# Kernel tuning notes

Measured on AMD Instinct MI355X. Metric: run time of the kernel, lower is better.

Reference implementation:

```python
import jax, jax.numpy as jnp
import numpy as np

B, C_IN, C_OUT, H, W, K, NK = 16, 256, 256, 64, 64, 3, 2
EPS = 1e-8


def setup_inputs() -> dict:
    key = jax.random.key(0)
    k1, k2, k3, k4 = jax.random.split(key, 4)
    x = jax.random.normal(k1, (B, C_IN, H, W), dtype=jnp.float32)
    mod = jax.random.normal(k2, (B, C_IN), dtype=jnp.float32)
    kernel_mod = jax.random.normal(k3, (B, NK), dtype=jnp.float32)
    # kernel bank: [num_conv_kernels, dim_out, dim_in, k, k] (kaiming-ish scale)
    weights = jax.random.normal(k4, (NK, C_OUT, C_IN, K, K), dtype=jnp.float32) / np.sqrt(C_IN * K * K)
    gamma = jnp.ones((C_OUT,), dtype=jnp.float32)
    return {"x": x, "mod": mod, "kernel_mod": kernel_mod, "weights": weights, "gamma": gamma}


def _block(x, mod, kernel_mod, weights, gamma):
    # adaptive kernel selection: softmax-mix the kernel bank per sample
    attn = jax.nn.softmax(kernel_mod, axis=-1)                       # [b, n]
    w = jnp.einsum('bn,noikl->boikl', attn, weights)                 # [b, o, i, k, k]
    # style modulation over input channels
    w = w * (mod[:, None, :, None, None] + 1.0)
    # demodulation
    denom = jnp.clip(jnp.sum(w * w, axis=(2, 3, 4), keepdims=True), EPS)
    w = w * jax.lax.rsqrt(denom)
    # per-sample conv (groups=b trick in torch) -> vmap over batch
    def conv_one(fmap, wb):
        return jax.lax.conv_general_dilated(
            fmap[None], wb, window_strides=(1, 1), padding='SAME',
            dimension_numbers=('NCHW', 'OIHW', 'NCHW'))[0]
    y = jax.vmap(conv_one)(x, w)                                     # [b, o, h, w]
    # RMSNorm over channel dim: F.normalize(x, dim=1) * gamma * sqrt(dim)
    norm = jnp.sqrt(jnp.sum(y * y, axis=1, keepdims=True))
    y = y / jnp.maximum(norm, 1e-12)
    y = y * gamma[None, :, None, None] * (gamma.shape[0] ** 0.5)
    # SiLU
    return y * jax.nn.sigmoid(y)


def reference(x, mod, kernel_mod, weights, gamma):
    return _block(x, mod, kernel_mod, weights, gamma)
```

## Files before the change

kernel.cpp:

```cpp
#include <hip/hip_runtime.h>
#include <math.h>


typedef __attribute__((ext_vector_type(8))) short short8;
typedef __attribute__((ext_vector_type(16))) float f32x16;

#define GLL16(src, dst)                                                       \
  __builtin_amdgcn_global_load_lds(                                           \
      (const __attribute__((address_space(1))) unsigned int*)(src),           \
      (__attribute__((address_space(3))) unsigned int*)(dst), 16, 0, 0)

static __device__ __forceinline__ unsigned short f2bf(float v) {
  union { float f; unsigned u; } u;
  u.f = v;
  unsigned r = u.u + 0x7FFF + ((u.u >> 16) & 1);
  return (unsigned short)(r >> 16);
}

__global__ __launch_bounds__(256) void wprep(
    const float* __restrict__ mod, const float* __restrict__ kmod,
    const float* __restrict__ weights, unsigned short* __restrict__ wq) {
  int blk = blockIdx.x;
  int b = blk >> 5, oq = blk & 31;
  int t = threadIdx.x;
  int o_l = t >> 5, its = t & 31;
  int o = oq * 8 + o_l;

  float k0 = kmod[b * 2 + 0], k1 = kmod[b * 2 + 1];
  float mx = fmaxf(k0, k1);
  float e0 = expf(k0 - mx), e1 = expf(k1 - mx);
  float ai = 1.0f / (e0 + e1);
  float a0 = e0 * ai, a1 = e1 * ai;

  float wv[9][8];
  float s = 0.0f;
  const float* w0 = &weights[((size_t)o * 256 + its * 8) * 9];
  const float* w1 = w0 + 589824;
#pragma unroll
  for (int e = 0; e < 8; ++e) {
    float f = mod[b * 256 + its * 8 + e] + 1.0f;
#pragma unroll
    for (int j = 0; j < 9; ++j) {
      float v = (a0 * w0[e * 9 + j] + a1 * w1[e * 9 + j]) * f;
      wv[j][e] = v;
      s = fmaf(v, v, s);
    }
  }

  __shared__ float red[8][32];
  __shared__ float scl[8];
  red[o_l][its] = s;
  __syncthreads();
  if (t < 8) {
    float tot = 0.0f;
#pragma unroll
    for (int k = 0; k < 32; ++k) tot += red[t][k];
    scl[t] = rsqrtf(fmaxf(tot, 1e-8f));
  }
  __syncthreads();
  float sc = scl[o_l];

  int c = its >> 1, io = its & 1;
  int oh = o >> 7, mf = (o >> 5) & 3;
  int lane2 = (o & 31) + io * 32;
  size_t cbase = ((size_t)(b * 16 + c)) * 36864 + oh * 2048 + mf * 512 + lane2 * 8;
#pragma unroll
  for (int j = 0; j < 9; ++j) {
    short8 pk;
#pragma unroll
    for (int e = 0; e < 8; ++e) pk[e] = (short)f2bf(wv[j][e] * sc);
    *(short8*)(wq + cbase + j * 4096) = pk;
  }
}

__global__ __launch_bounds__(256) void xprep(
    const float* __restrict__ x, unsigned short* __restrict__ xq) {
  int blk = blockIdx.x;
  int rowp = blk % 66;
  int bc = blk / 66;
  int b = bc >> 4, c = bc & 15;
  int t = threadIdx.x;
  size_t obase = (size_t)blk * 1056;

  if (rowp == 0 || rowp == 65) {
    for (int idx = t; idx < 1056; idx += 256) xq[obase + idx] = 0;
    return;
  }
  __shared__ __align__(16) unsigned short xs2[1056];
  int row = rowp - 1;
  for (int idx = t; idx < 1056; idx += 256) xs2[idx] = 0;
  __syncthreads();
#pragma unroll
  for (int k = 0; k < 4; ++k) {
    int idx = t + k * 256;
    int il = idx >> 6, col = idx & 63;
    float v = x[(((size_t)b * 256 + c * 16 + il) * 64 + row) * 64 + col];
    xs2[(col + 1) * 16 + il] = f2bf(v);
  }
  __syncthreads();
  if (t < 132) *(short8*)(xq + obase + (size_t)t * 8) = *(const short8*)&xs2[t * 8];
}

__global__ __launch_bounds__(256, 1) void conv_fused(
    const unsigned short* __restrict__ xq, const unsigned short* __restrict__ wq,
    const float* __restrict__ gamma, float* __restrict__ out) {
  __shared__ __align__(16) unsigned short wsm[36864];
  __shared__ __align__(16) unsigned short xsm[2][8192];
  __shared__ float redl[1024];
  __shared__ float invs[256];
  __shared__ float gsm[256];

  int bid = blockIdx.x;
  int xcd = bid & 7;
  int kk = bid >> 3;
  int b = xcd * 2 + (kk >> 4);
  int rt = kk & 15;
  int r0 = rt * 4;

  int t = threadIdx.x;
  int w = t >> 6, lane = t & 63;
  int oh = w >> 1, pq = w & 1;
  int l31 = lane & 31, l5 = lane >> 5;

  gsm[t] = gamma[t];

  const char* aw = (const char*)wsm + oh * 4096 + lane * 16;
  const char* xb0 = (const char*)xsm[0] + ((2 * pq) * 66 + l31) * 32 + l5 * 16;
  const char* xb1 = (const char*)xsm[1] + ((2 * pq) * 66 + l31) * 32 + l5 * 16;

  f32x16 acc[4][4];
#pragma unroll
  for (int mf = 0; mf < 4; ++mf)
#pragma unroll
    for (int nf = 0; nf < 4; ++nf)
#pragma unroll
      for (int q = 0; q < 16; ++q) acc[mf][nf][q] = 0.f;

#define GLLL(cn)                                                               \
  _Pragma("unroll") for (int r = 0; r < 8; ++r) {                              \
    GLL16(wq + ((size_t)(b * 16 + (cn))) * 36864 + (r * 256 + t) * 8,          \
          &wsm[(r * 256 + t) * 8]);                                            \
  }
#define GLLH(cn)                                                               \
  _Pragma("unroll") for (int r = 0; r < 10; ++r) {                             \
    GLL16(wq + ((size_t)(b * 16 + (cn))) * 36864 + 16384 + (r * 256 + t) * 8,  \
          &wsm[16384 + (r * 256 + t) * 8]);                                    \
  }
#define GLLX(cn, nb)                                                           \
  _Pragma("unroll") for (int r = 0; r < 4; ++r) {                              \
    GLL16(xq + ((size_t)((b * 16 + (cn)) * 66 + r0)) * 1056 + (r * 256 + t) * 8, \
          &xsm[nb][(r * 256 + t) * 8]);                                        \
  }

#define TAP(T, xbp)                                                            \
  {                                                                            \
    short8 A[4], Bv[4];                                                        \
    _Pragma("unroll") for (int mf = 0; mf < 4; ++mf)                           \
        A[mf] = *(const short8*)(aw + (T) * 8192 + mf * 1024);                 \
    _Pragma("unroll") for (int r = 0; r < 2; ++r)                              \
        _Pragma("unroll") for (int h = 0; h < 2; ++h)                          \
            Bv[r * 2 + h] = *(const short8*)((xbp) + ((T) / 3) * 2112 +        \
                                             ((T) % 3) * 32 + r * 2112 +       \
                                             h * 1024);                        \
    _Pragma("unroll") for (int nf = 0; nf < 4; ++nf)                           \
        _Pragma("unroll") for (int mf = 0; mf < 4; ++mf)                       \
            acc[mf][nf] = __builtin_amdgcn_mfma_f32_32x32x16_bf16(             \
                A[mf], Bv[nf], acc[mf][nf], 0, 0, 0);                          \
  }

#define SBAR __builtin_amdgcn_sched_barrier(0)
#define LGKM0 asm volatile("s_waitcnt lgkmcnt(0)" ::: "memory")
#define VMC(n) asm volatile("s_waitcnt vmcnt(" #n ")" ::: "memory")
#define BAR __builtin_amdgcn_s_barrier()

  GLLL(0); GLLH(0); GLLX(0, 0);
  VMC(0);
  BAR;
  SBAR;

  for (int c = 0; c < 16; ++c) {
    const char* xbp = (c & 1) ? xb1 : xb0;
    TAP(0, xbp); TAP(1, xbp); TAP(2, xbp); TAP(3, xbp);
    LGKM0; SBAR;
    BAR;
    if (c < 15) {
      GLLL(c + 1); GLLX(c + 1, (c & 1) ^ 1);
      VMC(12); SBAR;
    }
    TAP(4, xbp); TAP(5, xbp); TAP(6, xbp); TAP(7, xbp); TAP(8, xbp);
    LGKM0; SBAR;
    BAR;
    if (c < 15) {
      GLLH(c + 1);
      VMC(10); SBAR;
    }
  }

#pragma unroll
  for (int r = 0; r < 2; ++r)
#pragma unroll
    for (int h = 0; h < 2; ++h) {
      int nf = r * 2 + h;
      float ps = 0.f;
#pragma unroll
      for (int mf = 0; mf < 4; ++mf)
#pragma unroll
        for (int q = 0; q < 16; ++q) {
          float v = acc[mf][nf][q];
          ps = fmaf(v, v, ps);
        }
      int px = (2 * pq + r) * 64 + h * 32 + l31;
      redl[(oh * 2 + l5) * 256 + px] = ps;
    }
  __syncthreads();
  {
    float ssum = redl[t] + redl[256 + t] + redl[512 + t] + redl[768 + t];
    invs[t] = 16.0f / fmaxf(sqrtf(ssum), 1e-12f);
  }
  __syncthreads();
  float iv4[4];
#pragma unroll
  for (int r = 0; r < 2; ++r)
#pragma unroll
    for (int h = 0; h < 2; ++h)
      iv4[r * 2 + h] = invs[(2 * pq + r) * 64 + h * 32 + l31];

#pragma unroll
  for (int mf = 0; mf < 4; ++mf)
#pragma unroll
    for (int q = 0; q < 16; ++q) {
      int o = oh * 128 + mf * 32 + (q & 3) + 8 * (q >> 2) + 4 * l5;
      float g = gsm[o];
      size_t ob = (((size_t)b * 256 + o) * 64);
#pragma unroll
      for (int r = 0; r < 2; ++r)
#pragma unroll
        for (int h = 0; h < 2; ++h) {
          float v = acc[mf][r * 2 + h][q] * iv4[r * 2 + h] * g;
          float sg = 1.0f / (1.0f + expf(-v));
          out[(ob + (r0 + 2 * pq + r)) * 64 + h * 32 + l31] = v * sg;
        }
    }
#undef GLLL
#undef GLLH
#undef GLLX
#undef TAP
#undef SBAR
#undef LGKM0
#undef VMC
#undef BAR
}

extern "C" void kernel_launch(void* const* d_in, const int* in_sizes, int n_in,
                              void* d_out, int out_size, void* d_ws, size_t ws_size,
                              hipStream_t stream) {
  const float* x = (const float*)d_in[0];
  const float* mod = (const float*)d_in[1];
  const float* kmod = (const float*)d_in[2];
  const float* weights = (const float*)d_in[3];
  const float* gamma = (const float*)d_in[4];
  float* out = (float*)d_out;

  unsigned short* xq = (unsigned short*)d_ws;
  unsigned short* wq = (unsigned short*)((char*)d_ws + 35684352);

  wprep<<<512, 256, 0, stream>>>(mod, kmod, weights, wq);
  xprep<<<16 * 16 * 66, 256, 0, stream>>>(x, xq);
  conv_fused<<<256, 256, 0, stream>>>(xq, wq, gamma, out);
}
```

Measured before the change: 124.2 us.

## Double conv block to 512 threads with per-wave pixel-row split

The fused conv kernel now runs 8 waves per block instead of 4. Each wave owns one output pixel row and half the output channels, so it holds 4x2 accumulator tiles instead of 4x4. The aim is to cut per-wave register pressure and give each SIMD two waves for latency hiding. In exchange, each wave reads the weight A-fragments from LDS for half as many MFMAs, which raises LDS read traffic. The prefetch waits also change from partial vmcnt counts to full vmcnt(0) waits before each barrier, which may shrink the overlap between global loads and MFMAs.

New measurement: 121.0 us (median of 2 runs). -2.6%, faster.

```diff
diff --git a/kernel.cpp b/kernel.cpp
--- a/kernel.cpp
+++ b/kernel.cpp
@@ -101,7 +101,7 @@
   if (t < 132) *(short8*)(xq + obase + (size_t)t * 8) = *(const short8*)&xs2[t * 8];
 }
 
-__global__ __launch_bounds__(256, 1) void conv_fused(
+__global__ __launch_bounds__(512, 2) void conv_fused(
     const unsigned short* __restrict__ xq, const unsigned short* __restrict__ wq,
     const float* __restrict__ gamma, float* __restrict__ out) {
   __shared__ __align__(16) unsigned short wsm[36864];
@@ -119,111 +119,103 @@
 
   int t = threadIdx.x;
   int w = t >> 6, lane = t & 63;
-  int oh = w >> 1, pq = w & 1;
+  int oh = w & 1, ps = w >> 1;
   int l31 = lane & 31, l5 = lane >> 5;
 
-  gsm[t] = gamma[t];
+  if (t < 256) gsm[t] = gamma[t];
 
   const char* aw = (const char*)wsm + oh * 4096 + lane * 16;
-  const char* xb0 = (const char*)xsm[0] + ((2 * pq) * 66 + l31) * 32 + l5 * 16;
-  const char* xb1 = (const char*)xsm[1] + ((2 * pq) * 66 + l31) * 32 + l5 * 16;
-
-  f32x16 acc[4][4];
+  const char* xb0 = (const char*)xsm[0] + (ps * 66 + l31) * 32 + l5 * 16;
+  const char* xb1 = (const char*)xsm[1] + (ps * 66 + l31) * 32 + l5 * 16;
+
+  f32x16 acc[4][2];
 #pragma unroll
   for (int mf = 0; mf < 4; ++mf)
 #pragma unroll
-    for (int nf = 0; nf < 4; ++nf)
-#pragma unroll
-      for (int q = 0; q < 16; ++q) acc[mf][nf][q] = 0.f;
+    for (int h = 0; h < 2; ++h)
+#pragma unroll
+      for (int q = 0; q < 16; ++q) acc[mf][h][q] = 0.f;
 
 #define GLLL(cn)                                                               \
-  _Pragma("unroll") for (int r = 0; r < 8; ++r) {                              \
-    GLL16(wq + ((size_t)(b * 16 + (cn))) * 36864 + (r * 256 + t) * 8,          \
-          &wsm[(r * 256 + t) * 8]);                                            \
+  _Pragma("unroll") for (int r = 0; r < 4; ++r) {                              \
+    GLL16(wq + ((size_t)(b * 16 + (cn))) * 36864 + (r * 512 + t) * 8,          \
+          &wsm[(r * 512 + t) * 8]);                                            \
   }
 #define GLLH(cn)                                                               \
-  _Pragma("unroll") for (int r = 0; r < 10; ++r) {                             \
-    GLL16(wq + ((size_t)(b * 16 + (cn))) * 36864 + 16384 + (r * 256 + t) * 8,  \
-          &wsm[16384 + (r * 256 + t) * 8]);                                    \
+  _Pragma("unroll") for (int r = 0; r < 5; ++r) {                              \
+    GLL16(wq + ((size_t)(b * 16 + (cn))) * 36864 + 16384 + (r * 512 + t) * 8,  \
+          &wsm[16384 + (r * 512 + t) * 8]);                                    \
   }
 #define GLLX(cn, nb)                                                           \
-  _Pragma("unroll") for (int r = 0; r < 4; ++r) {                              \
-    GLL16(xq + ((size_t)((b * 16 + (cn)) * 66 + r0)) * 1056 + (r * 256 + t) * 8, \
-          &xsm[nb][(r * 256 + t) * 8]);                                        \
+  _Pragma("unroll") for (int r = 0; r < 2; ++r) {                              \
+    GLL16(xq + ((size_t)((b * 16 + (cn)) * 66 + r0)) * 1056 + (r * 512 + t) * 8, \
+          &xsm[nb][(r * 512 + t) * 8]);                                        \
   }
 
 #define TAP(T, xbp)                                                            \
   {                                                                            \
-    short8 A[4], Bv[4];                                                        \
+    short8 A[4], Bv[2];                                                        \
     _Pragma("unroll") for (int mf = 0; mf < 4; ++mf)                           \
         A[mf] = *(const short8*)(aw + (T) * 8192 + mf * 1024);                 \
-    _Pragma("unroll") for (int r = 0; r < 2; ++r)                              \
-        _Pragma("unroll") for (int h = 0; h < 2; ++h)                          \
-            Bv[r * 2 + h] = *(const short8*)((xbp) + ((T) / 3) * 2112 +        \
-                                             ((T) % 3) * 32 + r * 2112 +       \
-                                             h * 1024);                        \
-    _Pragma("unroll") for (int nf = 0; nf < 4; ++nf)                           \
+    _Pragma("unroll") for (int h = 0; h < 2; ++h)                              \
+        Bv[h] = *(const short8*)((xbp) + ((T) / 3) * 2112 + ((T) % 3) * 32 +   \
+                                 h * 1024);                                    \
+    _Pragma("unroll") for (int h = 0; h < 2; ++h)                              \
         _Pragma("unroll") for (int mf = 0; mf < 4; ++mf)                       \
-            acc[mf][nf] = __builtin_amdgcn_mfma_f32_32x32x16_bf16(             \
-                A[mf], Bv[nf], acc[mf][nf], 0, 0, 0);                          \
+            acc[mf][h] = __builtin_amdgcn_mfma_f32_32x32x16_bf16(              \
+                A[mf], Bv[h], acc[mf][h], 0, 0, 0);                            \
   }
 
 #define SBAR __builtin_amdgcn_sched_barrier(0)
 #define LGKM0 asm volatile("s_waitcnt lgkmcnt(0)" ::: "memory")
-#define VMC(n) asm volatile("s_waitcnt vmcnt(" #n ")" ::: "memory")
+#define VM0 asm volatile("s_waitcnt vmcnt(0)" ::: "memory")
 #define BAR __builtin_amdgcn_s_barrier()
 
   GLLL(0); GLLH(0); GLLX(0, 0);
-  VMC(0);
+  VM0;
   BAR;
   SBAR;
 
   for (int c = 0; c < 16; ++c) {
     const char* xbp = (c & 1) ? xb1 : xb0;
     TAP(0, xbp); TAP(1, xbp); TAP(2, xbp); TAP(3, xbp);
-    LGKM0; SBAR;
+    LGKM0;
+    VM0;
+    SBAR;
     BAR;
-    if (c < 15) {
-      GLLL(c + 1); GLLX(c + 1, (c & 1) ^ 1);
-      VMC(12); SBAR;
-    }
+    SBAR;
+    if (c < 15) { GLLL(c + 1); GLLX(c + 1, (c & 1) ^ 1); }
     TAP(4, xbp); TAP(5, xbp); TAP(6, xbp); TAP(7, xbp); TAP(8, xbp);
-    LGKM0; SBAR;
+    LGKM0;
+    VM0;
+    SBAR;
     BAR;
-    if (c < 15) {
-      GLLH(c + 1);
-      VMC(10); SBAR;
-    }
-  }
-
-#pragma unroll
-  for (int r = 0; r < 2; ++r)
-#pragma unroll
-    for (int h = 0; h < 2; ++h) {
-      int nf = r * 2 + h;
-      float ps = 0.f;
-#pragma unroll
-      for (int mf = 0; mf < 4; ++mf)
-#pragma unroll
-        for (int q = 0; q < 16; ++q) {
-          float v = acc[mf][nf][q];
-          ps = fmaf(v, v, ps);
-        }
-      int px = (2 * pq + r) * 64 + h * 32 + l31;
-      redl[(oh * 2 + l5) * 256 + px] = ps;
-    }
-  __syncthreads();
-  {
+    SBAR;
+    if (c < 15) { GLLH(c + 1); }
+  }
+
+#pragma unroll
+  for (int h = 0; h < 2; ++h) {
+    float pssum = 0.f;
+#pragma unroll
+    for (int mf = 0; mf < 4; ++mf)
+#pragma unroll
+      for (int q = 0; q < 16; ++q) {
+        float v = acc[mf][h][q];
+        pssum = fmaf(v, v, pssum);
+      }
+    int px = ps * 64 + h * 32 + l31;
+    redl[(oh * 2 + l5) * 256 + px] = pssum;
+  }
+  __syncthreads();
+  if (t < 256) {
     float ssum = redl[t] + redl[256 + t] + redl[512 + t] + redl[768 + t];
     invs[t] = 16.0f / fmaxf(sqrtf(ssum), 1e-12f);
   }
   __syncthreads();
-  float iv4[4];
-#pragma unroll
-  for (int r = 0; r < 2; ++r)
-#pragma unroll
-    for (int h = 0; h < 2; ++h)
-      iv4[r * 2 + h] = invs[(2 * pq + r) * 64 + h * 32 + l31];
+  float iv2[2];
+#pragma unroll
+  for (int h = 0; h < 2; ++h) iv2[h] = invs[ps * 64 + h * 32 + l31];
 
 #pragma unroll
   for (int mf = 0; mf < 4; ++mf)
@@ -231,15 +223,13 @@
     for (int q = 0; q < 16; ++q) {
       int o = oh * 128 + mf * 32 + (q & 3) + 8 * (q >> 2) + 4 * l5;
       float g = gsm[o];
-      size_t ob = (((size_t)b * 256 + o) * 64);
-#pragma unroll
-      for (int r = 0; r < 2; ++r)
-#pragma unroll
-        for (int h = 0; h < 2; ++h) {
-          float v = acc[mf][r * 2 + h][q] * iv4[r * 2 + h] * g;
-          float sg = 1.0f / (1.0f + expf(-v));
-          out[(ob + (r0 + 2 * pq + r)) * 64 + h * 32 + l31] = v * sg;
-        }
+      size_t ob = ((size_t)b * 256 + o) * 64 + (r0 + ps);
+#pragma unroll
+      for (int h = 0; h < 2; ++h) {
+        float v = acc[mf][h][q] * iv2[h] * g;
+        float sg = 1.0f / (1.0f + expf(-v));
+        out[ob * 64 + h * 32 + l31] = v * sg;
+      }
     }
 #undef GLLL
 #undef GLLH
@@ -247,7 +237,7 @@
 #undef TAP
 #undef SBAR
 #undef LGKM0
-#undef VMC
+#undef VM0
 #undef BAR
 }
 
@@ -266,5 +256,5 @@
 
   wprep<<<512, 256, 0, stream>>>(mod, kmod, weights, wq);
   xprep<<<16 * 16 * 66, 256, 0, stream>>>(x, xq);
-  conv_fused<<<256, 256, 0, stream>>>(xq, wq, gamma, out);
-}
+  conv_fused<<<256, 512, 0, stream>>>(xq, wq, gamma, out);
+}
```
